# Performance work log

Measured on AMD Instinct MI355X. Metric: run time of the kernel, lower is better.

Reference implementation:

```python
import jax, jax.numpy as jnp
import numpy as np

B, N, K, C = 4, 8192, 16, 64
HID, OUT = 128, 128


def setup_inputs() -> dict:
    key = jax.random.key(0)
    ks = jax.random.split(key, 8)
    f = jax.random.normal(ks[0], (B, N, C), dtype=jnp.float32)
    knn_idx = jax.random.randint(ks[1], (B, N, K), 0, N, dtype=jnp.int32)
    W1 = jax.random.normal(ks[2], (3 * C, HID), dtype=jnp.float32) * (1.0 / np.sqrt(3 * C))
    b1 = jnp.zeros((HID,), dtype=jnp.float32)
    W2 = jax.random.normal(ks[3], (HID, HID), dtype=jnp.float32) * (1.0 / np.sqrt(HID))
    b2 = jnp.zeros((HID,), dtype=jnp.float32)
    W3 = jax.random.normal(ks[4], (HID, OUT), dtype=jnp.float32) * 0.05  # init.normal_(std=0.05)
    b3 = jnp.zeros((OUT,), dtype=jnp.float32)  # init.zeros_
    return {"f": f, "knn_idx": knn_idx, "W1": W1, "b1": b1, "W2": W2, "b2": b2, "W3": W3, "b3": b3}


def reference(f, knn_idx, W1, b1, W2, b2, W3, b3):
    # knn_group: gather neighbor features -> [B, N, k, C]
    knn_feat = jax.vmap(lambda fb, ib: fb[ib])(f, knn_idx)
    f_tiled = jnp.broadcast_to(f[:, :, None, :], knn_feat.shape)  # [B,N,k,C]
    x = jnp.concatenate([f_tiled, knn_feat, knn_feat - f_tiled], axis=-1)  # [B,N,k,3C]
    x = jax.nn.relu(jnp.einsum('bnkc,ch->bnkh', x, W1) + b1)
    x = jax.nn.relu(jnp.einsum('bnkh,hg->bnkg', x, W2) + b2)
    x = jnp.max(x, axis=2)  # max-pool over k -> [B,N,HID]
    return jnp.einsum('bnh,ho->bno', x, W3) + b3
```

## Files before the change

### kernel.cpp

```cpp
#include <hip/hip_runtime.h>


#define BB 4
#define NN 8192
#define KK 16
#define CC 64
#define HH 128

typedef _Float16 f16;
typedef __fp16 h16x2 __attribute__((ext_vector_type(2)));
typedef _Float16 f16x8 __attribute__((ext_vector_type(8)));
typedef float f32x4 __attribute__((ext_vector_type(4)));

#define MFMA16(a, b, c) __builtin_amdgcn_mfma_f32_16x16x32_f16(a, b, c, 0, 0, 0)

static __device__ __forceinline__ f16x8 cvt8(f32x4 a0, f32x4 a1) {
  h16x2 c0 = __builtin_amdgcn_cvt_pkrtz(a0[0], a0[1]);
  h16x2 c1 = __builtin_amdgcn_cvt_pkrtz(a0[2], a0[3]);
  h16x2 c2 = __builtin_amdgcn_cvt_pkrtz(a1[0], a1[1]);
  h16x2 c3 = __builtin_amdgcn_cvt_pkrtz(a1[2], a1[3]);
  f16x8 v;
  v[0] = (f16)c0[0]; v[1] = (f16)c0[1]; v[2] = (f16)c1[0]; v[3] = (f16)c1[1];
  v[4] = (f16)c2[0]; v[5] = (f16)c2[1]; v[6] = (f16)c3[0]; v[7] = (f16)c3[1];
  return v;
}

static __device__ __forceinline__ void lds_barrier() {
  asm volatile("s_waitcnt lgkmcnt(0)" ::: "memory");
  __builtin_amdgcn_s_barrier();
  __builtin_amdgcn_sched_barrier(0);
}

__global__ void prep_pack(const float* __restrict__ W1, const float* __restrict__ W2,
                          const float* __restrict__ W3, f16* __restrict__ ws) {
  int fid = blockIdx.x;
  int l = threadIdx.x;
  int g = l >> 4, r = l & 15;
  f16x8 v;
#pragma unroll
  for (int j = 0; j < 8; ++j) {
    int kl = 16 * (j >> 2) + 4 * g + (j & 3);
    float x;
    if (fid < 32) {
      int ht = fid >> 2, kt = fid & 3, h = ht * 16 + r;
      if (kt < 2) {
        int k = kt * 32 + kl;
        x = W1[(64 + k) * HH + h] + W1[(128 + k) * HH + h];
      } else {
        int k = (kt - 2) * 32 + kl;
        x = W1[k * HH + h] - W1[(128 + k) * HH + h];
      }
    } else if (fid < 64) {
      int t = fid - 32, h2t = t >> 2, kt = t & 3;
      x = W2[(kt * 32 + kl) * HH + h2t * 16 + r];
    } else {
      int t = fid - 64, ot = t >> 2, kt = t & 3;
      x = W3[(kt * 32 + kl) * HH + ot * 16 + r];
    }
    v[j] = (f16)x;
  }
  *(f16x8*)(ws + (size_t)fid * 512 + l * 8) = v;
}

__global__ __launch_bounds__(512, 4) void knn_main(
    const float* __restrict__ f, const int* __restrict__ knn,
    const float* __restrict__ b1, const float* __restrict__ b2,
    const float* __restrict__ b3, const f16* __restrict__ ws,
    float* __restrict__ out) {
  extern __shared__ char smem[];
  f16* wbuf = (f16*)smem;
  f16* pooled = wbuf + 64 * 512;

  const int tid = threadIdx.x;
  const int wave = tid >> 6, lane = tid & 63;
  const int g = lane >> 4, r = lane & 15;

  const int wg = (blockIdx.x & 7) * 256 + (blockIdx.x >> 3);
  const int b = wg >> 9;
  const int n0 = (wg & 511) * 16;
  const float* fb = f + (size_t)b * NN * CC;
  const int p0 = wave * 2;

  int nidx[2];
#pragma unroll
  for (int pp = 0; pp < 2; ++pp)
    nidx[pp] = knn[(size_t)(b * NN + n0 + p0 + pp) * KK + r];

  f16x8 st[8];
#pragma unroll
  for (int i = 0; i < 8; ++i)
    st[i] = *(const f16x8*)(ws + (size_t)(i * 512 + tid) * 8);
#pragma unroll
  for (int i = 0; i < 8; ++i)
    *(f16x8*)(wbuf + (size_t)(i * 512 + tid) * 8) = st[i];

  f16x8 bf[2][4];
#pragma unroll
  for (int pp = 0; pp < 2; ++pp) {
    const float* fown = fb + (size_t)(n0 + p0 + pp) * CC;
#pragma unroll
    for (int kt = 2; kt < 4; ++kt) {
      f32x4 a0 = *(const f32x4*)(fown + (kt - 2) * 32 + 4 * g);
      f32x4 a1 = *(const f32x4*)(fown + (kt - 2) * 32 + 4 * g + 16);
      bf[pp][kt] = cvt8(a0, a1);
    }
  }

  f32x4 rawN[2][2][2];
#pragma unroll
  for (int pp = 0; pp < 2; ++pp) {
    const float* frow = fb + (size_t)nidx[pp] * CC;
#pragma unroll
    for (int kt = 0; kt < 2; ++kt) {
      rawN[pp][kt][0] = *(const f32x4*)(frow + kt * 32 + 4 * g);
      rawN[pp][kt][1] = *(const f32x4*)(frow + kt * 32 + 4 * g + 16);
    }
  }

  lds_barrier();

#pragma unroll
  for (int pp = 0; pp < 2; ++pp)
#pragma unroll
    for (int kt = 0; kt < 2; ++kt)
      bf[pp][kt] = cvt8(rawN[pp][kt][0], rawN[pp][kt][1]);

  f16x8 h1f[2][4];
#pragma unroll
  for (int ht = 0; ht < 8; ++ht) {
    f32x4 acc[2] = {{0.f, 0.f, 0.f, 0.f}, {0.f, 0.f, 0.f, 0.f}};
#pragma unroll
    for (int kt = 0; kt < 4; ++kt) {
      f16x8 wfrag = *(const f16x8*)(wbuf + (size_t)(ht * 4 + kt) * 512 + lane * 8);
      acc[0] = MFMA16(wfrag, bf[0][kt], acc[0]);
      acc[1] = MFMA16(wfrag, bf[1][kt], acc[1]);
    }
    f32x4 b1v = *(const f32x4*)(b1 + ht * 16 + g * 4);
#pragma unroll
    for (int pp = 0; pp < 2; ++pp) {
      float x0 = acc[pp][0] + b1v[0]; x0 = x0 > 0.f ? x0 : 0.f;
      float x1 = acc[pp][1] + b1v[1]; x1 = x1 > 0.f ? x1 : 0.f;
      float x2 = acc[pp][2] + b1v[2]; x2 = x2 > 0.f ? x2 : 0.f;
      float x3 = acc[pp][3] + b1v[3]; x3 = x3 > 0.f ? x3 : 0.f;
      h16x2 lo = __builtin_amdgcn_cvt_pkrtz(x0, x1);
      h16x2 hi = __builtin_amdgcn_cvt_pkrtz(x2, x3);
      h1f[pp][ht >> 1][(ht & 1) * 4 + 0] = (f16)lo[0];
      h1f[pp][ht >> 1][(ht & 1) * 4 + 1] = (f16)lo[1];
      h1f[pp][ht >> 1][(ht & 1) * 4 + 2] = (f16)hi[0];
      h1f[pp][ht >> 1][(ht & 1) * 4 + 3] = (f16)hi[1];
    }
  }

#pragma unroll
  for (int h2t = 0; h2t < 8; ++h2t) {
    f32x4 c0 = {0.f, 0.f, 0.f, 0.f}, c1 = {0.f, 0.f, 0.f, 0.f};
#pragma unroll
    for (int kt = 0; kt < 4; ++kt) {
      f16x8 w2f = *(const f16x8*)(wbuf + (size_t)(32 + h2t * 4 + kt) * 512 + lane * 8);
      c0 = MFMA16(h1f[0][kt], w2f, c0);
      c1 = MFMA16(h1f[1][kt], w2f, c1);
    }
    float b2v = b2[h2t * 16 + r];
#pragma unroll
    for (int pp = 0; pp < 2; ++pp) {
      f32x4 cc = pp ? c1 : c0;
      float m = fmaxf(fmaxf(cc[0], cc[1]), fmaxf(cc[2], cc[3]));
      m = fmaxf(m, __shfl_xor(m, 16, 64));
      m = fmaxf(m, __shfl_xor(m, 32, 64));
      float x = m + b2v;
      f16 pv = (f16)(x > 0.f ? x : 0.f);
      if (g == 0) {
        pooled[(h2t >> 1) * 512 + ((r >> 2) * 16 + p0 + pp) * 8 +
               (h2t & 1) * 4 + (r & 3)] = pv;
      }
    }
  }

  f16x8 w3f[4];
#pragma unroll
  for (int kt = 0; kt < 4; ++kt)
    w3f[kt] = *(const f16x8*)(ws + (size_t)(64 + wave * 4 + kt) * 512 + lane * 8);

  lds_barrier();

  {
    f32x4 a3 = {0.f, 0.f, 0.f, 0.f};
#pragma unroll
    for (int kt = 0; kt < 4; ++kt) {
      f16x8 pf = *(const f16x8*)(pooled + kt * 512 + lane * 8);
      a3 = MFMA16(w3f[kt], pf, a3);
    }
    f32x4 b3v = *(const f32x4*)(b3 + wave * 16 + g * 4);
    f32x4 o;
#pragma unroll
    for (int i = 0; i < 4; ++i) o[i] = a3[i] + b3v[i];
    *(f32x4*)(out + ((size_t)b * NN + n0 + r) * HH + wave * 16 + g * 4) = o;
  }
}

extern "C" void kernel_launch(void* const* d_in, const int* in_sizes, int n_in,
                              void* d_out, int out_size, void* d_ws, size_t ws_size,
                              hipStream_t stream) {
  const float* f = (const float*)d_in[0];
  const int* knn = (const int*)d_in[1];
  const float* W1 = (const float*)d_in[2];
  const float* b1 = (const float*)d_in[3];
  const float* W2 = (const float*)d_in[4];
  const float* b2 = (const float*)d_in[5];
  const float* W3 = (const float*)d_in[6];
  const float* b3 = (const float*)d_in[7];
  float* outp = (float*)d_out;
  f16* wsp = (f16*)d_ws;

  (void)hipFuncSetAttribute((const void*)knn_main,
                            hipFuncAttributeMaxDynamicSharedMemorySize, 69632);

  prep_pack<<<96, 64, 0, stream>>>(W1, W2, W3, wsp);
  knn_main<<<(BB * NN) / 16, 512, 69632, stream>>>(f, knn, b1, b2, b3, wsp, outp);
}
```

Measured before the change: 53.32 us.

## Make blocks persistent over four point tiles with prefetch of next gathers

Each block now handles 64 points in four iterations of 16 instead of one tile, so the 64 KB weight staging into LDS is amortized across four tiles. The own-feature and neighbor-feature loads for the next tile are issued before the W3 stage and final barrier, overlapping global gather latency with compute. The grid shrinks by a factor of four (512 blocks), which reduces parallelism and latency hiding across blocks, and an extra barrier per iteration is added.

```diff
diff --git a/kernel.cpp b/kernel.cpp
--- a/kernel.cpp
+++ b/kernel.cpp
@@ -6,6 +6,7 @@
 #define KK 16
 #define CC 64
 #define HH 128
+#define ITERS 4
 
 typedef _Float16 f16;
 typedef __fp16 h16x2 __attribute__((ext_vector_type(2)));
@@ -75,17 +76,12 @@
   const int wave = tid >> 6, lane = tid & 63;
   const int g = lane >> 4, r = lane & 15;
 
-  const int wg = (blockIdx.x & 7) * 256 + (blockIdx.x >> 3);
-  const int b = wg >> 9;
-  const int n0 = (wg & 511) * 16;
+  const int wg = (blockIdx.x & 7) * 64 + (blockIdx.x >> 3);
+  const int b = wg >> 7;
+  const int nbase = (wg & 127) * 64;
   const float* fb = f + (size_t)b * NN * CC;
   const int p0 = wave * 2;
 
-  int nidx[2];
-#pragma unroll
-  for (int pp = 0; pp < 2; ++pp)
-    nidx[pp] = knn[(size_t)(b * NN + n0 + p0 + pp) * KK + r];
-
   f16x8 st[8];
 #pragma unroll
   for (int i = 0; i < 8; ++i)
@@ -94,107 +90,149 @@
   for (int i = 0; i < 8; ++i)
     *(f16x8*)(wbuf + (size_t)(i * 512 + tid) * 8) = st[i];
 
-  f16x8 bf[2][4];
+  int nidx[2];
+#pragma unroll
+  for (int pp = 0; pp < 2; ++pp)
+    nidx[pp] = knn[(size_t)(b * NN + nbase + p0 + pp) * KK + r];
+
+  f32x4 rawO[2][2][2];
+  f32x4 rawN[2][2][2];
 #pragma unroll
   for (int pp = 0; pp < 2; ++pp) {
-    const float* fown = fb + (size_t)(n0 + p0 + pp) * CC;
-#pragma unroll
-    for (int kt = 2; kt < 4; ++kt) {
-      f32x4 a0 = *(const f32x4*)(fown + (kt - 2) * 32 + 4 * g);
-      f32x4 a1 = *(const f32x4*)(fown + (kt - 2) * 32 + 4 * g + 16);
-      bf[pp][kt] = cvt8(a0, a1);
-    }
-  }
-
-  f32x4 rawN[2][2][2];
+    const float* fo = fb + (size_t)(nbase + p0 + pp) * CC;
+#pragma unroll
+    for (int kt = 0; kt < 2; ++kt) {
+      rawO[pp][kt][0] = *(const f32x4*)(fo + kt * 32 + 4 * g);
+      rawO[pp][kt][1] = *(const f32x4*)(fo + kt * 32 + 4 * g + 16);
+    }
+  }
 #pragma unroll
   for (int pp = 0; pp < 2; ++pp) {
-    const float* frow = fb + (size_t)nidx[pp] * CC;
+    const float* fn = fb + (size_t)nidx[pp] * CC;
 #pragma unroll
     for (int kt = 0; kt < 2; ++kt) {
-      rawN[pp][kt][0] = *(const f32x4*)(frow + kt * 32 + 4 * g);
-      rawN[pp][kt][1] = *(const f32x4*)(frow + kt * 32 + 4 * g + 16);
+      rawN[pp][kt][0] = *(const f32x4*)(fn + kt * 32 + 4 * g);
+      rawN[pp][kt][1] = *(const f32x4*)(fn + kt * 32 + 4 * g + 16);
     }
   }
 
   lds_barrier();
 
-#pragma unroll
-  for (int pp = 0; pp < 2; ++pp)
-#pragma unroll
-    for (int kt = 0; kt < 2; ++kt)
-      bf[pp][kt] = cvt8(rawN[pp][kt][0], rawN[pp][kt][1]);
-
-  f16x8 h1f[2][4];
-#pragma unroll
-  for (int ht = 0; ht < 8; ++ht) {
-    f32x4 acc[2] = {{0.f, 0.f, 0.f, 0.f}, {0.f, 0.f, 0.f, 0.f}};
-#pragma unroll
-    for (int kt = 0; kt < 4; ++kt) {
-      f16x8 wfrag = *(const f16x8*)(wbuf + (size_t)(ht * 4 + kt) * 512 + lane * 8);
-      acc[0] = MFMA16(wfrag, bf[0][kt], acc[0]);
-      acc[1] = MFMA16(wfrag, bf[1][kt], acc[1]);
-    }
-    f32x4 b1v = *(const f32x4*)(b1 + ht * 16 + g * 4);
+  for (int it = 0; it < ITERS; ++it) {
+    const int n0 = nbase + it * 16;
+    const int itn = (it < ITERS - 1) ? it + 1 : it;
+
+    int nidxN[2];
+#pragma unroll
+    for (int pp = 0; pp < 2; ++pp)
+      nidxN[pp] = knn[(size_t)(b * NN + nbase + itn * 16 + p0 + pp) * KK + r];
+
+    f16x8 bf[2][4];
 #pragma unroll
     for (int pp = 0; pp < 2; ++pp) {
-      float x0 = acc[pp][0] + b1v[0]; x0 = x0 > 0.f ? x0 : 0.f;
-      float x1 = acc[pp][1] + b1v[1]; x1 = x1 > 0.f ? x1 : 0.f;
-      float x2 = acc[pp][2] + b1v[2]; x2 = x2 > 0.f ? x2 : 0.f;
-      float x3 = acc[pp][3] + b1v[3]; x3 = x3 > 0.f ? x3 : 0.f;
-      h16x2 lo = __builtin_amdgcn_cvt_pkrtz(x0, x1);
-      h16x2 hi = __builtin_amdgcn_cvt_pkrtz(x2, x3);
-      h1f[pp][ht >> 1][(ht & 1) * 4 + 0] = (f16)lo[0];
-      h1f[pp][ht >> 1][(ht & 1) * 4 + 1] = (f16)lo[1];
-      h1f[pp][ht >> 1][(ht & 1) * 4 + 2] = (f16)hi[0];
-      h1f[pp][ht >> 1][(ht & 1) * 4 + 3] = (f16)hi[1];
-    }
-  }
-
-#pragma unroll
-  for (int h2t = 0; h2t < 8; ++h2t) {
-    f32x4 c0 = {0.f, 0.f, 0.f, 0.f}, c1 = {0.f, 0.f, 0.f, 0.f};
-#pragma unroll
-    for (int kt = 0; kt < 4; ++kt) {
-      f16x8 w2f = *(const f16x8*)(wbuf + (size_t)(32 + h2t * 4 + kt) * 512 + lane * 8);
-      c0 = MFMA16(h1f[0][kt], w2f, c0);
-      c1 = MFMA16(h1f[1][kt], w2f, c1);
-    }
-    float b2v = b2[h2t * 16 + r];
+#pragma unroll
+      for (int kt = 0; kt < 2; ++kt)
+        bf[pp][kt] = cvt8(rawN[pp][kt][0], rawN[pp][kt][1]);
+#pragma unroll
+      for (int kt = 2; kt < 4; ++kt)
+        bf[pp][kt] = cvt8(rawO[pp][kt - 2][0], rawO[pp][kt - 2][1]);
+    }
+
+    f16x8 h1f[2][4];
+#pragma unroll
+    for (int ht = 0; ht < 8; ++ht) {
+      f32x4 acc[2] = {{0.f, 0.f, 0.f, 0.f}, {0.f, 0.f, 0.f, 0.f}};
+#pragma unroll
+      for (int kt = 0; kt < 4; ++kt) {
+        f16x8 wfrag = *(const f16x8*)(wbuf + (size_t)(ht * 4 + kt) * 512 + lane * 8);
+        acc[0] = MFMA16(wfrag, bf[0][kt], acc[0]);
+        acc[1] = MFMA16(wfrag, bf[1][kt], acc[1]);
+      }
+      f32x4 b1v = *(const f32x4*)(b1 + ht * 16 + g * 4);
+#pragma unroll
+      for (int pp = 0; pp < 2; ++pp) {
+        float x0 = acc[pp][0] + b1v[0]; x0 = x0 > 0.f ? x0 : 0.f;
+        float x1 = acc[pp][1] + b1v[1]; x1 = x1 > 0.f ? x1 : 0.f;
+        float x2 = acc[pp][2] + b1v[2]; x2 = x2 > 0.f ? x2 : 0.f;
+        float x3 = acc[pp][3] + b1v[3]; x3 = x3 > 0.f ? x3 : 0.f;
+        h16x2 lo = __builtin_amdgcn_cvt_pkrtz(x0, x1);
+        h16x2 hi = __builtin_amdgcn_cvt_pkrtz(x2, x3);
+        h1f[pp][ht >> 1][(ht & 1) * 4 + 0] = (f16)lo[0];
+        h1f[pp][ht >> 1][(ht & 1) * 4 + 1] = (f16)lo[1];
+        h1f[pp][ht >> 1][(ht & 1) * 4 + 2] = (f16)hi[0];
+        h1f[pp][ht >> 1][(ht & 1) * 4 + 3] = (f16)hi[1];
+      }
+    }
+
+#pragma unroll
+    for (int h2t = 0; h2t < 8; ++h2t) {
+      f32x4 c0 = {0.f, 0.f, 0.f, 0.f}, c1 = {0.f, 0.f, 0.f, 0.f};
+#pragma unroll
+      for (int kt = 0; kt < 4; ++kt) {
+        f16x8 w2f = *(const f16x8*)(wbuf + (size_t)(32 + h2t * 4 + kt) * 512 + lane * 8);
+        c0 = MFMA16(h1f[0][kt], w2f, c0);
+        c1 = MFMA16(h1f[1][kt], w2f, c1);
+      }
+      float b2v = b2[h2t * 16 + r];
+#pragma unroll
+      for (int pp = 0; pp < 2; ++pp) {
+        f32x4 cc = pp ? c1 : c0;
+        float m = fmaxf(fmaxf(cc[0], cc[1]), fmaxf(cc[2], cc[3]));
+        m = fmaxf(m, __shfl_xor(m, 16, 64));
+        m = fmaxf(m, __shfl_xor(m, 32, 64));
+        float x = m + b2v;
+        f16 pv = (f16)(x > 0.f ? x : 0.f);
+        if (g == 0) {
+          pooled[(h2t >> 1) * 512 + ((r >> 2) * 16 + p0 + pp) * 8 +
+                 (h2t & 1) * 4 + (r & 3)] = pv;
+        }
+      }
+    }
+
 #pragma unroll
     for (int pp = 0; pp < 2; ++pp) {
-      f32x4 cc = pp ? c1 : c0;
-      float m = fmaxf(fmaxf(cc[0], cc[1]), fmaxf(cc[2], cc[3]));
-      m = fmaxf(m, __shfl_xor(m, 16, 64));
-      m = fmaxf(m, __shfl_xor(m, 32, 64));
-      float x = m + b2v;
-      f16 pv = (f16)(x > 0.f ? x : 0.f);
-      if (g == 0) {
-        pooled[(h2t >> 1) * 512 + ((r >> 2) * 16 + p0 + pp) * 8 +
-               (h2t & 1) * 4 + (r & 3)] = pv;
-      }
-    }
-  }
-
-  f16x8 w3f[4];
-#pragma unroll
-  for (int kt = 0; kt < 4; ++kt)
-    w3f[kt] = *(const f16x8*)(ws + (size_t)(64 + wave * 4 + kt) * 512 + lane * 8);
-
-  lds_barrier();
-
-  {
-    f32x4 a3 = {0.f, 0.f, 0.f, 0.f};
-#pragma unroll
-    for (int kt = 0; kt < 4; ++kt) {
-      f16x8 pf = *(const f16x8*)(pooled + kt * 512 + lane * 8);
-      a3 = MFMA16(w3f[kt], pf, a3);
-    }
-    f32x4 b3v = *(const f32x4*)(b3 + wave * 16 + g * 4);
-    f32x4 o;
-#pragma unroll
-    for (int i = 0; i < 4; ++i) o[i] = a3[i] + b3v[i];
-    *(f32x4*)(out + ((size_t)b * NN + n0 + r) * HH + wave * 16 + g * 4) = o;
+      const float* fo = fb + (size_t)(nbase + itn * 16 + p0 + pp) * CC;
+#pragma unroll
+      for (int kt = 0; kt < 2; ++kt) {
+        rawO[pp][kt][0] = *(const f32x4*)(fo + kt * 32 + 4 * g);
+        rawO[pp][kt][1] = *(const f32x4*)(fo + kt * 32 + 4 * g + 16);
+      }
+    }
+#pragma unroll
+    for (int pp = 0; pp < 2; ++pp) {
+      const float* fn = fb + (size_t)nidxN[pp] * CC;
+#pragma unroll
+      for (int kt = 0; kt < 2; ++kt) {
+        rawN[pp][kt][0] = *(const f32x4*)(fn + kt * 32 + 4 * g);
+        rawN[pp][kt][1] = *(const f32x4*)(fn + kt * 32 + 4 * g + 16);
+      }
+    }
+
+    f16x8 w3f[4];
+#pragma unroll
+    for (int kt = 0; kt < 4; ++kt)
+      w3f[kt] = *(const f16x8*)(ws + (size_t)(64 + wave * 4 + kt) * 512 + lane * 8);
+
+    lds_barrier();
+
+    {
+      f32x4 a3 = {0.f, 0.f, 0.f, 0.f};
+#pragma unroll
+      for (int kt = 0; kt < 4; ++kt) {
+        f16x8 pf = *(const f16x8*)(pooled + kt * 512 + lane * 8);
+        a3 = MFMA16(w3f[kt], pf, a3);
+      }
+      f32x4 b3v = *(const f32x4*)(b3 + wave * 16 + g * 4);
+      f32x4 o;
+#pragma unroll
+      for (int i = 0; i < 4; ++i) o[i] = a3[i] + b3v[i];
+      *(f32x4*)(out + ((size_t)b * NN + n0 + r) * HH + wave * 16 + g * 4) = o;
+    }
+
+    lds_barrier();
+
+    nidx[0] = nidxN[0];
+    nidx[1] = nidxN[1];
   }
 }
 
@@ -216,5 +254,5 @@
                             hipFuncAttributeMaxDynamicSharedMemorySize, 69632);
 
   prep_pack<<<96, 64, 0, stream>>>(W1, W2, W3, wsp);
-  knn_main<<<(BB * NN) / 16, 512, 69632, stream>>>(f, knn, b1, b2, b3, wsp, outp);
-}
+  knn_main<<<(BB * NN) / 64, 512, 69632, stream>>>(f, knn, b1, b2, b3, wsp, outp);
+}
```

New measurement: 92.88 us. +74.2%, slower.

## Hoist per-point self-feature term of layer 1 out of neighbor loop

Applied to the files above, without the earlier changes.

Splits the first layer so the center-point contribution (W1a - W1c applied to f) is computed once per point with one MFMA per wave and stored in LDS as fp32, instead of being recomputed for each of the 16 neighbors. The per-neighbor layer-1 GEMM shrinks from K=128 to K=64, and LDS weight staging drops from 64 to 48 fragments. The weight-packing kernel is also relaunched with 512-thread blocks. This adds an extra LDS buffer and dependence on the barrier for the per-point term.

```diff
diff --git a/kernel.cpp b/kernel.cpp
--- a/kernel.cpp
+++ b/kernel.cpp
@@ -33,26 +33,23 @@
 
 __global__ void prep_pack(const float* __restrict__ W1, const float* __restrict__ W2,
                           const float* __restrict__ W3, f16* __restrict__ ws) {
-  int fid = blockIdx.x;
-  int l = threadIdx.x;
+  int fid = blockIdx.x * 8 + (threadIdx.x >> 6);
+  int l = threadIdx.x & 63;
   int g = l >> 4, r = l & 15;
   f16x8 v;
 #pragma unroll
   for (int j = 0; j < 8; ++j) {
     int kl = 16 * (j >> 2) + 4 * g + (j & 3);
     float x;
-    if (fid < 32) {
-      int ht = fid >> 2, kt = fid & 3, h = ht * 16 + r;
-      if (kt < 2) {
-        int k = kt * 32 + kl;
-        x = W1[(64 + k) * HH + h] + W1[(128 + k) * HH + h];
-      } else {
-        int k = (kt - 2) * 32 + kl;
-        x = W1[k * HH + h] - W1[(128 + k) * HH + h];
-      }
+    if (fid < 16) {
+      int ht = fid >> 1, kt = fid & 1, h = ht * 16 + r, k = kt * 32 + kl;
+      x = W1[(64 + k) * HH + h] + W1[(128 + k) * HH + h];
+    } else if (fid < 48) {
+      int t = fid - 16, h2t = t >> 2, kt = t & 3;
+      x = W2[(kt * 32 + kl) * HH + h2t * 16 + r];
     } else if (fid < 64) {
-      int t = fid - 32, h2t = t >> 2, kt = t & 3;
-      x = W2[(kt * 32 + kl) * HH + h2t * 16 + r];
+      int t = fid - 48, ht = t >> 1, kt = t & 1, h = ht * 16 + r, k = kt * 32 + kl;
+      x = W1[k * HH + h] - W1[(128 + k) * HH + h];
     } else {
       int t = fid - 64, ot = t >> 2, kt = t & 3;
       x = W3[(kt * 32 + kl) * HH + ot * 16 + r];
@@ -69,7 +66,8 @@
     float* __restrict__ out) {
   extern __shared__ char smem[];
   f16* wbuf = (f16*)smem;
-  f16* pooled = wbuf + 64 * 512;
+  float* fabuf = (float*)(wbuf + 48 * 512);
+  f16* pooled = (f16*)(fabuf + 16 * 132);
 
   const int tid = threadIdx.x;
   const int wave = tid >> 6, lane = tid & 63;
@@ -86,39 +84,54 @@
   for (int pp = 0; pp < 2; ++pp)
     nidx[pp] = knn[(size_t)(b * NN + n0 + p0 + pp) * KK + r];
 
-  f16x8 st[8];
-#pragma unroll
-  for (int i = 0; i < 8; ++i)
+  const float* fo = fb + (size_t)(n0 + r) * CC;
+  f32x4 rawF[2][2];
+#pragma unroll
+  for (int kt = 0; kt < 2; ++kt) {
+    rawF[kt][0] = *(const f32x4*)(fo + kt * 32 + 4 * g);
+    rawF[kt][1] = *(const f32x4*)(fo + kt * 32 + 4 * g + 16);
+  }
+  f16x8 aw[2];
+#pragma unroll
+  for (int kt = 0; kt < 2; ++kt)
+    aw[kt] = *(const f16x8*)(ws + (size_t)(48 + wave * 2 + kt) * 512 + lane * 8);
+
+  f16x8 st[6];
+#pragma unroll
+  for (int i = 0; i < 6; ++i)
     st[i] = *(const f16x8*)(ws + (size_t)(i * 512 + tid) * 8);
 #pragma unroll
-  for (int i = 0; i < 8; ++i)
+  for (int i = 0; i < 6; ++i)
     *(f16x8*)(wbuf + (size_t)(i * 512 + tid) * 8) = st[i];
 
-  f16x8 bf[2][4];
+  f32x4 rawN[2][2][2];
 #pragma unroll
   for (int pp = 0; pp < 2; ++pp) {
-    const float* fown = fb + (size_t)(n0 + p0 + pp) * CC;
-#pragma unroll
-    for (int kt = 2; kt < 4; ++kt) {
-      f32x4 a0 = *(const f32x4*)(fown + (kt - 2) * 32 + 4 * g);
-      f32x4 a1 = *(const f32x4*)(fown + (kt - 2) * 32 + 4 * g + 16);
-      bf[pp][kt] = cvt8(a0, a1);
-    }
-  }
-
-  f32x4 rawN[2][2][2];
-#pragma unroll
-  for (int pp = 0; pp < 2; ++pp) {
-    const float* frow = fb + (size_t)nidx[pp] * CC;
+    const float* fn = fb + (size_t)nidx[pp] * CC;
 #pragma unroll
     for (int kt = 0; kt < 2; ++kt) {
-      rawN[pp][kt][0] = *(const f32x4*)(frow + kt * 32 + 4 * g);
-      rawN[pp][kt][1] = *(const f32x4*)(frow + kt * 32 + 4 * g + 16);
-    }
+      rawN[pp][kt][0] = *(const f32x4*)(fn + kt * 32 + 4 * g);
+      rawN[pp][kt][1] = *(const f32x4*)(fn + kt * 32 + 4 * g + 16);
+    }
+  }
+
+  {
+    f32x4 acc = {0.f, 0.f, 0.f, 0.f};
+#pragma unroll
+    for (int kt = 0; kt < 2; ++kt) {
+      f16x8 bfa = cvt8(rawF[kt][0], rawF[kt][1]);
+      acc = MFMA16(aw[kt], bfa, acc);
+    }
+    f32x4 b1v = *(const f32x4*)(b1 + wave * 16 + g * 4);
+    f32x4 fa;
+#pragma unroll
+    for (int i = 0; i < 4; ++i) fa[i] = acc[i] + b1v[i];
+    *(f32x4*)(fabuf + r * 132 + wave * 16 + g * 4) = fa;
   }
 
   lds_barrier();
 
+  f16x8 bf[2][2];
 #pragma unroll
   for (int pp = 0; pp < 2; ++pp)
 #pragma unroll
@@ -130,18 +143,20 @@
   for (int ht = 0; ht < 8; ++ht) {
     f32x4 acc[2] = {{0.f, 0.f, 0.f, 0.f}, {0.f, 0.f, 0.f, 0.f}};
 #pragma unroll
-    for (int kt = 0; kt < 4; ++kt) {
-      f16x8 wfrag = *(const f16x8*)(wbuf + (size_t)(ht * 4 + kt) * 512 + lane * 8);
+    for (int kt = 0; kt < 2; ++kt) {
+      f16x8 wfrag = *(const f16x8*)(wbuf + (size_t)(ht * 2 + kt) * 512 + lane * 8);
       acc[0] = MFMA16(wfrag, bf[0][kt], acc[0]);
       acc[1] = MFMA16(wfrag, bf[1][kt], acc[1]);
     }
-    f32x4 b1v = *(const f32x4*)(b1 + ht * 16 + g * 4);
+    f32x4 fa0 = *(const f32x4*)(fabuf + (p0 + 0) * 132 + ht * 16 + g * 4);
+    f32x4 fa1 = *(const f32x4*)(fabuf + (p0 + 1) * 132 + ht * 16 + g * 4);
 #pragma unroll
     for (int pp = 0; pp < 2; ++pp) {
-      float x0 = acc[pp][0] + b1v[0]; x0 = x0 > 0.f ? x0 : 0.f;
-      float x1 = acc[pp][1] + b1v[1]; x1 = x1 > 0.f ? x1 : 0.f;
-      float x2 = acc[pp][2] + b1v[2]; x2 = x2 > 0.f ? x2 : 0.f;
-      float x3 = acc[pp][3] + b1v[3]; x3 = x3 > 0.f ? x3 : 0.f;
+      const f32x4& fa = pp ? fa1 : fa0;
+      float x0 = acc[pp][0] + fa[0]; x0 = x0 > 0.f ? x0 : 0.f;
+      float x1 = acc[pp][1] + fa[1]; x1 = x1 > 0.f ? x1 : 0.f;
+      float x2 = acc[pp][2] + fa[2]; x2 = x2 > 0.f ? x2 : 0.f;
+      float x3 = acc[pp][3] + fa[3]; x3 = x3 > 0.f ? x3 : 0.f;
       h16x2 lo = __builtin_amdgcn_cvt_pkrtz(x0, x1);
       h16x2 hi = __builtin_amdgcn_cvt_pkrtz(x2, x3);
       h1f[pp][ht >> 1][(ht & 1) * 4 + 0] = (f16)lo[0];
@@ -156,7 +171,7 @@
     f32x4 c0 = {0.f, 0.f, 0.f, 0.f}, c1 = {0.f, 0.f, 0.f, 0.f};
 #pragma unroll
     for (int kt = 0; kt < 4; ++kt) {
-      f16x8 w2f = *(const f16x8*)(wbuf + (size_t)(32 + h2t * 4 + kt) * 512 + lane * 8);
+      f16x8 w2f = *(const f16x8*)(wbuf + (size_t)(16 + h2t * 4 + kt) * 512 + lane * 8);
       c0 = MFMA16(h1f[0][kt], w2f, c0);
       c1 = MFMA16(h1f[1][kt], w2f, c1);
     }
@@ -213,8 +228,8 @@
   f16* wsp = (f16*)d_ws;
 
   (void)hipFuncSetAttribute((const void*)knn_main,
-                            hipFuncAttributeMaxDynamicSharedMemorySize, 69632);
-
-  prep_pack<<<96, 64, 0, stream>>>(W1, W2, W3, wsp);
-  knn_main<<<(BB * NN) / 16, 512, 69632, stream>>>(f, knn, b1, b2, b3, wsp, outp);
-}
+                            hipFuncAttributeMaxDynamicSharedMemorySize, 61696);
+
+  prep_pack<<<12, 512, 0, stream>>>(W1, W2, W3, wsp);
+  knn_main<<<(BB * NN) / 16, 512, 61696, stream>>>(f, knn, b1, b2, b3, wsp, outp);
+}
```

Measured after the change: 53.74 us. Within noise of the previous version (+0.8%).
